# Optimization experiments

Measured on AMD Instinct MI355X. Metric: run time of the kernel, lower is better.

## Reference

```python
import jax, jax.numpy as jnp
import numpy as np

B, D_MODEL, N, H = 4, 256, 2048, 4
HEAD_DIM = D_MODEL // H  # 64


def _rotate_half(x):
    # x: [..., d] with d even; pairs (x1, x2) -> (-x2, x1)
    x = x.reshape(x.shape[:-1] + (x.shape[-1] // 2, 2))
    x1, x2 = x[..., 0], x[..., 1]
    return jnp.stack((-x2, x1), axis=-1).reshape(x.shape[:-2] + (-1,))


def _apply_rope(freqs, t):
    # freqs: [2, n, d] (cos, sin); t: [b, h, n, d]
    return t * freqs[0] + _rotate_half(t) * freqs[1]


def setup_inputs() -> dict:
    key = jax.random.key(0)
    ks = jax.random.split(key, 12)
    s = 0.02
    inp = {
        "query": jax.random.normal(ks[0], (B, D_MODEL, N), jnp.float32),
        "key": jax.random.normal(ks[1], (B, D_MODEL, N), jnp.float32),
        "value": jax.random.normal(ks[2], (B, D_MODEL, N), jnp.float32),
        "encoding": jax.random.normal(ks[3], (2, N, HEAD_DIM), jnp.float32),
        "Wq": jax.random.normal(ks[4], (D_MODEL, D_MODEL), jnp.float32) * s,
        "bq": jnp.zeros((D_MODEL,), jnp.float32),
        "Wk": jax.random.normal(ks[5], (D_MODEL, D_MODEL), jnp.float32) * s,
        "bk": jnp.zeros((D_MODEL,), jnp.float32),
        "Wv": jax.random.normal(ks[6], (D_MODEL, D_MODEL), jnp.float32) * s,
        "bv": jnp.zeros((D_MODEL,), jnp.float32),
        "Wm": jax.random.normal(ks[7], (D_MODEL, D_MODEL), jnp.float32) * s,
        "bm": jnp.zeros((D_MODEL,), jnp.float32),
    }
    return inp


def _proj(W, b, x):
    # 1x1 Conv1d == channel matmul: x [b, c_in, n] -> [b, c_out, n]
    return jnp.einsum('oi,bin->bon', W, x) + b[None, :, None]


def reference(query, key, value, encoding, Wq, bq, Wk, bk, Wv, bv, Wm, bm):
    b = query.shape[0]
    # project and split channels into (head_dim, heads): [b, d, h, n]
    q = _proj(Wq, bq, query).reshape(b, HEAD_DIM, H, -1)
    k = _proj(Wk, bk, key).reshape(b, HEAD_DIM, H, -1)
    v = _proj(Wv, bv, value).reshape(b, HEAD_DIM, H, -1)
    # RoPE on [b, h, n, d] layout
    q = jnp.transpose(_apply_rope(encoding, jnp.transpose(q, (0, 2, 3, 1))), (0, 3, 1, 2))
    k = jnp.transpose(_apply_rope(encoding, jnp.transpose(k, (0, 2, 3, 1))), (0, 3, 1, 2))
    # attention: scores [b, h, n, m]
    scores = jnp.einsum('bdhn,bdhm->bhnm', q, k) / jnp.sqrt(jnp.float32(HEAD_DIM))
    prob = jax.nn.softmax(scores, axis=-1)
    x = jnp.einsum('bhnm,bdhm->bdhn', prob, v)
    x = x.reshape(b, HEAD_DIM * H, -1)
    return _proj(Wm, bm, x)
```

## Files before the change

kernel.cpp:

```cpp
#include <hip/hip_runtime.h>
#include <stdint.h>

#define NSEQ 2048

typedef __attribute__((ext_vector_type(4))) float f32x4;
typedef __attribute__((ext_vector_type(8))) short s16x8;
typedef _Float16 f16x8 __attribute__((ext_vector_type(8)));
typedef _Float16 h16x2 __attribute__((ext_vector_type(2)));
typedef unsigned int u32;
typedef __attribute__((ext_vector_type(2))) unsigned int u32x2;

#define OFF_PO  0u
#define OFF_M   16777216u
#define OFF_L   17301504u
#define OFF_QR  17825792u
#define OFF_KR  22020096u
#define OFF_VT  26214400u
#define OFF_W   30408704u

__device__ __forceinline__ short f2h(float f) {
  _Float16 h = (_Float16)f;
  return __builtin_bit_cast(short, h);
}
__device__ __forceinline__ float h2f(short s) {
  return (float)__builtin_bit_cast(_Float16, s);
}
__device__ __forceinline__ int swz128(int row, int slot) {
  return row * 128 + ((slot ^ (row & 7)) << 4);
}
#define MFMA(a, b, c) __builtin_amdgcn_mfma_f32_16x16x32_f16(a, b, c, 0, 0, 0)

__global__ void k_convw(const float* __restrict__ Wq, const float* __restrict__ Wk,
                        const float* __restrict__ Wv, const float* __restrict__ Wm,
                        char* __restrict__ ws) {
  int o = blockIdx.x, which = blockIdx.y, i = threadIdx.x;
  const float* src = which == 0 ? Wq : which == 1 ? Wk : which == 2 ? Wv : Wm;
  short* dst = (short*)(ws + OFF_W) + which * 65536;
  float val = (which < 3) ? src[o * 256 + i] : src[o * 256 + ((i & 63) << 2) + (i >> 6)];
  dst[o * 256 + i] = f2h(val);
}

__global__ __launch_bounds__(256) void k_proj(const float* __restrict__ q,
    const float* __restrict__ k, const float* __restrict__ v,
    const float* __restrict__ enc, const float* __restrict__ bq,
    const float* __restrict__ bk, const float* __restrict__ bv, char* __restrict__ ws) {
  int hid = blockIdx.x + 32 * (blockIdx.y + 4 * blockIdx.z);
  int fm = (hid & 7) * 192 + (hid >> 3);
  int yo = fm & 3, xn = (fm >> 2) & 31, z = fm >> 7;
  int proj = z >> 2, b = z & 3;
  const float* xs = proj == 0 ? q : (proj == 1 ? k : v);
  const short* W = (const short*)(ws + OFF_W) + proj * 65536;
  int o0 = yo * 64, n0 = xn * 64;
  __shared__ short As[64 * 64], Bs[64 * 64];
  __shared__ float ftile[64][65];
  int t = threadIdx.x, lane = t & 63, g = lane >> 4, c = lane & 15, wave = t >> 6;
  int wr = wave >> 1, wc = wave & 1;
  int row = t >> 2, seg = t & 3;
  int nl = t & 63, ib = (t >> 6) * 16;
  f32x4 acc[2][2] = {};
  for (int kk = 0; kk < 4; ++kk) {
    int koff = kk * 64;
    __syncthreads();
    const short* wsrc = &W[(o0 + row) * 256 + koff];
    s16x8 wa0 = *(const s16x8*)(wsrc + seg * 8);
    s16x8 wa1 = *(const s16x8*)(wsrc + 32 + seg * 8);
#pragma unroll
    for (int r = 0; r < 16; ++r)
      ftile[ib + r][nl] = xs[(b * 256 + koff + ib + r) * 2048 + n0 + nl];
    *(s16x8*)((char*)As + swz128(row, seg))     = wa0;
    *(s16x8*)((char*)As + swz128(row, 4 + seg)) = wa1;
    __syncthreads();
    int ic = seg * 16;
    short hb[16];
#pragma unroll
    for (int j = 0; j < 16; ++j) hb[j] = f2h(ftile[ic + j][row]);
    *(s16x8*)((char*)Bs + swz128(row, ic >> 3))       = *(const s16x8*)&hb[0];
    *(s16x8*)((char*)Bs + swz128(row, (ic >> 3) + 1)) = *(const s16x8*)&hb[8];
    __syncthreads();
#pragma unroll
    for (int ks = 0; ks < 2; ++ks) {
      f16x8 af[2], bfr[2];
#pragma unroll
      for (int f = 0; f < 2; ++f) {
        af[f]  = *(const f16x8*)((char*)As + swz128(wr * 32 + f * 16 + c, ks * 4 + g));
        bfr[f] = *(const f16x8*)((char*)Bs + swz128(wc * 32 + f * 16 + c, ks * 4 + g));
      }
#pragma unroll
      for (int i = 0; i < 2; ++i)
#pragma unroll
        for (int j = 0; j < 2; ++j)
          acc[i][j] = MFMA(af[i], bfr[j], acc[i][j]);
    }
  }
  const float* bias = proj == 0 ? bq : (proj == 1 ? bk : bv);
  if (proj < 2) {
    short* dst0 = (short*)(ws + (proj == 0 ? OFF_QR : OFF_KR));
    float scale = proj == 0 ? 0.18033688f : 1.0f;
    float sgn = (g & 1) ? 1.0f : -1.0f;
#pragma unroll
    for (int i = 0; i < 2; ++i) {
      int ob = o0 + wr * 32 + i * 16 + g * 4;
      int d = ob >> 2;
#pragma unroll
      for (int j = 0; j < 2; ++j) {
        int n = n0 + wc * 32 + j * 16 + c;
        float cv = enc[n * 64 + d], sv = enc[131072 + n * 64 + d];
#pragma unroll
        for (int r = 0; r < 4; ++r) {
          float val = acc[i][j][r] + bias[ob + r];
          float par = __shfl_xor(val, 16, 64);
          float res = (val * cv + sgn * par * sv) * scale;
          dst0[((b * 4 + r) * 2048 + n) * 64 + d] = f2h(res);
        }
      }
    }
  } else {
    short* dst = (short*)(ws + OFF_VT);
#pragma unroll
    for (int i = 0; i < 2; ++i) {
      int ob = o0 + wr * 32 + i * 16 + g * 4;
      int d = ob >> 2;
#pragma unroll
      for (int j = 0; j < 2; ++j) {
        int n = n0 + wc * 32 + j * 16 + c;
#pragma unroll
        for (int r = 0; r < 4; ++r) {
          float val = acc[i][j][r] + bias[ob + r];
          dst[((b * 4 + r) * 64 + d) * 2048 + n] = f2h(val);
        }
      }
    }
  }
}

__global__ __launch_bounds__(256, 4) void k_attn(char* __restrict__ ws) {
  int bh = blockIdx.y, ms = blockIdx.z;
  int t = threadIdx.x, wave = t >> 6, lane = t & 63, g = lane >> 4, c = lane & 15;
  int nw = blockIdx.x * 64 + wave * 16;
  const short* Q = (const short*)(ws + OFF_QR) + bh * 131072;
  const short* K = (const short*)(ws + OFF_KR) + bh * 131072;
  const short* V = (const short*)(ws + OFF_VT) + bh * 131072;
  __shared__ short Ks[64 * 64], Vs[64 * 64], Ps[4][16 * 64];
  char* Pb = (char*)Ps[wave];
  f16x8 qf0 = *(const f16x8*)&Q[(nw + c) * 64 + g * 8];
  f16x8 qf1 = *(const f16x8*)&Q[(nw + c) * 64 + 32 + g * 8];
  f32x4 po[4] = {};
  float mrun = -1e30f, lrun = 0.f;
  int sr = t >> 3, sl = t & 7;
  const int mb = ms * 512;
  int bsrc = g * 16 + g * 4;

  s16x8 RA[4], RB[4];
  auto LD = [&](int m0, s16x8* R) {
    R[0] = *(const s16x8*)&K[(m0 + sr) * 64 + sl * 8];
    R[1] = *(const s16x8*)&K[(m0 + sr + 32) * 64 + sl * 8];
    R[2] = *(const s16x8*)&V[sr * 2048 + m0 + sl * 8];
    R[3] = *(const s16x8*)&V[(sr + 32) * 2048 + m0 + sl * 8];
  };
  auto ST = [&](const s16x8* R) {
    *(s16x8*)((char*)Ks + swz128(sr, sl))      = R[0];
    *(s16x8*)((char*)Ks + swz128(sr + 32, sl)) = R[1];
    *(s16x8*)((char*)Vs + swz128(sr, sl))      = R[2];
    *(s16x8*)((char*)Vs + swz128(sr + 32, sl)) = R[3];
  };
  auto COMPUTE = [&]() {
    f32x4 s[4] = {};
    __builtin_amdgcn_s_setprio(1);
#pragma unroll
    for (int fj = 0; fj < 4; ++fj) {
      f16x8 k0 = *(const f16x8*)((char*)Ks + swz128(fj * 16 + c, g));
      f16x8 k1 = *(const f16x8*)((char*)Ks + swz128(fj * 16 + c, 4 + g));
      s[fj] = MFMA(k0, qf0, s[fj]);
      s[fj] = MFMA(k1, qf1, s[fj]);
    }
    __builtin_amdgcn_s_setprio(0);
    float t0 = fmaxf(fmaxf(s[0][0], s[0][1]), fmaxf(s[0][2], s[0][3]));
    float t1 = fmaxf(fmaxf(s[1][0], s[1][1]), fmaxf(s[1][2], s[1][3]));
    float t2 = fmaxf(fmaxf(s[2][0], s[2][1]), fmaxf(s[2][2], s[2][3]));
    float t3 = fmaxf(fmaxf(s[3][0], s[3][1]), fmaxf(s[3][2], s[3][3]));
    float rmax = fmaxf(fmaxf(t0, t1), fmaxf(t2, t3));
    rmax = fmaxf(rmax, __shfl_xor(rmax, 16, 64));
    rmax = fmaxf(rmax, __shfl_xor(rmax, 32, 64));
    if (__any(rmax > mrun + 11.5f)) {
      float nm = fmaxf(mrun, rmax);
      float corr = exp2f(mrun - nm);
      mrun = nm;
      lrun *= corr;
#pragma unroll
      for (int r = 0; r < 4; ++r) {
        float corr_r = __shfl(corr, bsrc + r, 64);
#pragma unroll
        for (int fd = 0; fd < 4; ++fd) po[fd][r] *= corr_r;
      }
    }
    float p[4][4], rs = 0.f;
#pragma unroll
    for (int fj = 0; fj < 4; ++fj) {
      f32x4 pv;
#pragma unroll
      for (int r = 0; r < 4; ++r) {
        pv[r] = exp2f(s[fj][r] - mrun);
        p[fj][r] = pv[r];
      }
      rs += (pv[0] + pv[1]) + (pv[2] + pv[3]);
    }
    rs += __shfl_xor(rs, 16, 64);
    rs += __shfl_xor(rs, 32, 64);
    lrun += rs;
#pragma unroll
    for (int fj = 0; fj < 4; ++fj) {
      u32 lo = __builtin_bit_cast(u32, __builtin_amdgcn_cvt_pkrtz(p[fj][0], p[fj][1]));
      u32 hi = __builtin_bit_cast(u32, __builtin_amdgcn_cvt_pkrtz(p[fj][2], p[fj][3]));
      u32x2 pk; pk[0] = lo; pk[1] = hi;
      int slot = (fj * 16 + g * 4) >> 3;
      *(u32x2*)(Pb + swz128(c, slot) + (g & 1) * 8) = pk;
    }
    asm volatile("s_waitcnt lgkmcnt(0)" ::: "memory");
    __builtin_amdgcn_sched_barrier(0);
    f16x8 pa0 = *(const f16x8*)(Pb + swz128(c, g));
    f16x8 pa1 = *(const f16x8*)(Pb + swz128(c, 4 + g));
    __builtin_amdgcn_s_setprio(1);
#pragma unroll
    for (int fd = 0; fd < 4; ++fd) {
      int dd = fd * 16 + c;
      f16x8 vb0 = *(const f16x8*)((char*)Vs + swz128(dd, g));
      f16x8 vb1 = *(const f16x8*)((char*)Vs + swz128(dd, 4 + g));
      po[fd] = MFMA(pa0, vb0, po[fd]);
      po[fd] = MFMA(pa1, vb1, po[fd]);
    }
    __builtin_amdgcn_s_setprio(0);
  };

  LD(mb, RA);
  for (int tt = 0; tt < 8; tt += 2) {
    __syncthreads();
    ST(RA);
    LD(mb + (tt + 1) * 64, RB);
    __syncthreads();
    COMPUTE();
    __syncthreads();
    ST(RB);
    if (tt + 2 < 8) LD(mb + (tt + 2) * 64, RA);
    __syncthreads();
    COMPUTE();
  }

  short* PO = (short*)(ws + OFF_PO);
  float* Mm = (float*)(ws + OFF_M);
  float* Ll = (float*)(ws + OFF_L);
  int base = (ms * 16 + bh) * 2048;
  float li[4];
#pragma unroll
  for (int r = 0; r < 4; ++r) li[r] = 1.0f / __shfl(lrun, bsrc + r, 64);
  asm volatile("s_waitcnt lgkmcnt(0)" ::: "memory");
  __builtin_amdgcn_sched_barrier(0);
#pragma unroll
  for (int fd = 0; fd < 4; ++fd) {
    int d = fd * 16 + c;
#pragma unroll
    for (int r = 0; r < 4; ++r)
      *(short*)(Pb + swz128(g * 4 + r, d >> 3) + (d & 7) * 2) = f2h(po[fd][r] * li[r]);
  }
  asm volatile("s_waitcnt lgkmcnt(0)" ::: "memory");
  __builtin_amdgcn_sched_barrier(0);
  int rr = lane >> 2, ds = (lane & 3) * 16;
  s16x8 v0 = *(const s16x8*)(Pb + swz128(rr, ds >> 3));
  s16x8 v1 = *(const s16x8*)(Pb + swz128(rr, (ds >> 3) + 1));
  *(s16x8*)&PO[(base + nw + rr) * 64 + ds]     = v0;
  *(s16x8*)&PO[(base + nw + rr) * 64 + ds + 8] = v1;
  if (g == 0) {
    Mm[base + nw + c] = mrun;
    Ll[base + nw + c] = lrun;
  }
}

__global__ __launch_bounds__(256) void k_final(const float* __restrict__ bm,
    float* __restrict__ out, char* __restrict__ ws) {
  int hid = blockIdx.x + 64 * (blockIdx.y + 4 * blockIdx.z);
  int fm = (hid & 7) * 128 + (hid >> 3);
  int yo = fm & 3, xn = (fm >> 2) & 63, b = fm >> 8;
  int o0 = yo * 64, n0 = xn * 32;
  const short* Wf = (const short*)(ws + OFF_W) + 3 * 65536;
  const short* PO = (const short*)(ws + OFF_PO);
  const float* Mm = (const float*)(ws + OFF_M);
  const float* Ll = (const float*)(ws + OFF_L);
  __shared__ short As[64 * 64], Bs[32 * 64];
  int t = threadIdx.x, lane = t & 63, g = lane >> 4, c = lane & 15, wave = t >> 6;
  int wr = wave >> 1, wc = wave & 1;
  int arow = t >> 2, aseg = t & 3;
  int brow = t >> 3, bseg = t & 7;
  f32x4 acc[2] = {};
  for (int kk = 0; kk < 4; ++kk) {
    __syncthreads();
    const short* wsrc = &Wf[(o0 + arow) * 256 + kk * 64];
    *(s16x8*)((char*)As + swz128(arow, aseg))     = *(const s16x8*)(wsrc + aseg * 8);
    *(s16x8*)((char*)As + swz128(arow, 4 + aseg)) = *(const s16x8*)(wsrc + 32 + aseg * 8);
    int bh = b * 4 + kk;
    int nr = n0 + brow;
    float m0 = Mm[(0 * 16 + bh) * 2048 + nr], l0 = Ll[(0 * 16 + bh) * 2048 + nr];
    float m1 = Mm[(1 * 16 + bh) * 2048 + nr], l1 = Ll[(1 * 16 + bh) * 2048 + nr];
    float m2 = Mm[(2 * 16 + bh) * 2048 + nr], l2 = Ll[(2 * 16 + bh) * 2048 + nr];
    float m3 = Mm[(3 * 16 + bh) * 2048 + nr], l3 = Ll[(3 * 16 + bh) * 2048 + nr];
    float M = fmaxf(fmaxf(m0, m1), fmaxf(m2, m3));
    float w0 = l0 * exp2f(m0 - M), w1 = l1 * exp2f(m1 - M);
    float w2 = l2 * exp2f(m2 - M), w3 = l3 * exp2f(m3 - M);
    float inv = 1.f / (w0 + w1 + w2 + w3);
    w0 *= inv; w1 *= inv; w2 *= inv; w3 *= inv;
    s16x8 a0 = *(const s16x8*)&PO[((0 * 16 + bh) * 2048 + nr) * 64 + bseg * 8];
    s16x8 a1 = *(const s16x8*)&PO[((1 * 16 + bh) * 2048 + nr) * 64 + bseg * 8];
    s16x8 a2 = *(const s16x8*)&PO[((2 * 16 + bh) * 2048 + nr) * 64 + bseg * 8];
    s16x8 a3 = *(const s16x8*)&PO[((3 * 16 + bh) * 2048 + nr) * 64 + bseg * 8];
    short hb[8];
#pragma unroll
    for (int j = 0; j < 8; ++j)
      hb[j] = f2h(w0 * h2f(a0[j]) + w1 * h2f(a1[j]) + w2 * h2f(a2[j]) + w3 * h2f(a3[j]));
    *(s16x8*)((char*)Bs + swz128(brow, bseg)) = *(const s16x8*)hb;
    __syncthreads();
#pragma unroll
    for (int ks = 0; ks < 2; ++ks) {
      f16x8 af[2], bfr;
#pragma unroll
      for (int f = 0; f < 2; ++f)
        af[f] = *(const f16x8*)((char*)As + swz128(wr * 32 + f * 16 + c, ks * 4 + g));
      bfr = *(const f16x8*)((char*)Bs + swz128(wc * 16 + c, ks * 4 + g));
#pragma unroll
      for (int i = 0; i < 2; ++i)
        acc[i] = MFMA(af[i], bfr, acc[i]);
    }
  }
#pragma unroll
  for (int i = 0; i < 2; ++i) {
    int ob = o0 + wr * 32 + i * 16 + g * 4;
    int n = n0 + wc * 16 + c;
#pragma unroll
    for (int r = 0; r < 4; ++r)
      out[(b * 256 + ob + r) * 2048 + n] = acc[i][r] + bm[ob + r];
  }
}

extern "C" void kernel_launch(void* const* d_in, const int* in_sizes, int n_in,
                              void* d_out, int out_size, void* d_ws, size_t ws_size,
                              hipStream_t stream) {
  (void)in_sizes; (void)n_in; (void)out_size; (void)ws_size;
  const float* q   = (const float*)d_in[0];
  const float* k   = (const float*)d_in[1];
  const float* v   = (const float*)d_in[2];
  const float* enc = (const float*)d_in[3];
  const float* Wq  = (const float*)d_in[4];
  const float* bq  = (const float*)d_in[5];
  const float* Wk  = (const float*)d_in[6];
  const float* bk  = (const float*)d_in[7];
  const float* Wv  = (const float*)d_in[8];
  const float* bv  = (const float*)d_in[9];
  const float* Wm  = (const float*)d_in[10];
  const float* bm  = (const float*)d_in[11];
  char* ws = (char*)d_ws;
  float* out = (float*)d_out;
  hipLaunchKernelGGL(k_convw, dim3(256, 4), dim3(256), 0, stream, Wq, Wk, Wv, Wm, ws);
  hipLaunchKernelGGL(k_proj, dim3(32, 4, 12), dim3(256), 0, stream, q, k, v, enc, bq, bk, bv, ws);
  hipLaunchKernelGGL(k_attn, dim3(32, 16, 4), dim3(256), 0, stream, ws);
  hipLaunchKernelGGL(k_final, dim3(64, 4, 4), dim3(256), 0, stream, bm, out, ws);
}
```

Before: 162.7 us.

## Read K/V fragments directly from global memory and remap attention blocks

Removes the shared-memory staging of K and V tiles, together with the register double-buffer and the four block barriers per tile pair. Each wave now loads its MFMA operands straight from global memory and relies on L1/L2 for reuse across the four waves. The block index is remapped so that blocks of the same head and m-split are spread across XCD-interleaved launch order, and launch bounds are raised to allow more blocks per CU. The trade is more global and cache traffic per wave and exposed load latency in exchange for no barriers, less LDS use and higher occupancy.

```diff
diff --git a/kernel.cpp b/kernel.cpp
--- a/kernel.cpp
+++ b/kernel.cpp
@@ -6,7 +6,6 @@
 typedef __attribute__((ext_vector_type(4))) float f32x4;
 typedef __attribute__((ext_vector_type(8))) short s16x8;
 typedef _Float16 f16x8 __attribute__((ext_vector_type(8)));
-typedef _Float16 h16x2 __attribute__((ext_vector_type(2)));
 typedef unsigned int u32;
 typedef __attribute__((ext_vector_type(2))) unsigned int u32x2;
 
@@ -133,43 +132,32 @@
   }
 }
 
-__global__ __launch_bounds__(256, 4) void k_attn(char* __restrict__ ws) {
-  int bh = blockIdx.y, ms = blockIdx.z;
+__global__ __launch_bounds__(256, 6) void k_attn(char* __restrict__ ws) {
+  int hid = blockIdx.x + 32 * (blockIdx.y + 16 * blockIdx.z);
+  int fm = (hid & 7) * 256 + (hid >> 3);
+  int qx = fm & 31, bh = (fm >> 5) & 15, ms = fm >> 9;
   int t = threadIdx.x, wave = t >> 6, lane = t & 63, g = lane >> 4, c = lane & 15;
-  int nw = blockIdx.x * 64 + wave * 16;
+  int nw = qx * 64 + wave * 16;
   const short* Q = (const short*)(ws + OFF_QR) + bh * 131072;
   const short* K = (const short*)(ws + OFF_KR) + bh * 131072;
   const short* V = (const short*)(ws + OFF_VT) + bh * 131072;
-  __shared__ short Ks[64 * 64], Vs[64 * 64], Ps[4][16 * 64];
+  __shared__ short Ps[4][16 * 64];
   char* Pb = (char*)Ps[wave];
   f16x8 qf0 = *(const f16x8*)&Q[(nw + c) * 64 + g * 8];
   f16x8 qf1 = *(const f16x8*)&Q[(nw + c) * 64 + 32 + g * 8];
   f32x4 po[4] = {};
   float mrun = -1e30f, lrun = 0.f;
-  int sr = t >> 3, sl = t & 7;
   const int mb = ms * 512;
   int bsrc = g * 16 + g * 4;
 
-  s16x8 RA[4], RB[4];
-  auto LD = [&](int m0, s16x8* R) {
-    R[0] = *(const s16x8*)&K[(m0 + sr) * 64 + sl * 8];
-    R[1] = *(const s16x8*)&K[(m0 + sr + 32) * 64 + sl * 8];
-    R[2] = *(const s16x8*)&V[sr * 2048 + m0 + sl * 8];
-    R[3] = *(const s16x8*)&V[(sr + 32) * 2048 + m0 + sl * 8];
-  };
-  auto ST = [&](const s16x8* R) {
-    *(s16x8*)((char*)Ks + swz128(sr, sl))      = R[0];
-    *(s16x8*)((char*)Ks + swz128(sr + 32, sl)) = R[1];
-    *(s16x8*)((char*)Vs + swz128(sr, sl))      = R[2];
-    *(s16x8*)((char*)Vs + swz128(sr + 32, sl)) = R[3];
-  };
-  auto COMPUTE = [&]() {
+  for (int tt = 0; tt < 8; ++tt) {
+    int m0 = mb + tt * 64;
     f32x4 s[4] = {};
     __builtin_amdgcn_s_setprio(1);
 #pragma unroll
     for (int fj = 0; fj < 4; ++fj) {
-      f16x8 k0 = *(const f16x8*)((char*)Ks + swz128(fj * 16 + c, g));
-      f16x8 k1 = *(const f16x8*)((char*)Ks + swz128(fj * 16 + c, 4 + g));
+      f16x8 k0 = *(const f16x8*)&K[(m0 + fj * 16 + c) * 64 + g * 8];
+      f16x8 k1 = *(const f16x8*)&K[(m0 + fj * 16 + c) * 64 + 32 + g * 8];
       s[fj] = MFMA(k0, qf0, s[fj]);
       s[fj] = MFMA(k1, qf1, s[fj]);
     }
@@ -223,26 +211,12 @@
 #pragma unroll
     for (int fd = 0; fd < 4; ++fd) {
       int dd = fd * 16 + c;
-      f16x8 vb0 = *(const f16x8*)((char*)Vs + swz128(dd, g));
-      f16x8 vb1 = *(const f16x8*)((char*)Vs + swz128(dd, 4 + g));
+      f16x8 vb0 = *(const f16x8*)&V[dd * 2048 + m0 + g * 8];
+      f16x8 vb1 = *(const f16x8*)&V[dd * 2048 + m0 + 32 + g * 8];
       po[fd] = MFMA(pa0, vb0, po[fd]);
       po[fd] = MFMA(pa1, vb1, po[fd]);
     }
     __builtin_amdgcn_s_setprio(0);
-  };
-
-  LD(mb, RA);
-  for (int tt = 0; tt < 8; tt += 2) {
-    __syncthreads();
-    ST(RA);
-    LD(mb + (tt + 1) * 64, RB);
-    __syncthreads();
-    COMPUTE();
-    __syncthreads();
-    ST(RB);
-    if (tt + 2 < 8) LD(mb + (tt + 2) * 64, RA);
-    __syncthreads();
-    COMPUTE();
   }
 
   short* PO = (short*)(ws + OFF_PO);
```

New measurement: 254.0 us. 1.56x slower.
